# Kernel optimization log

Hardware: AMD Instinct MI355X
Metric: run time of the kernel (lower is better)

The kernel has to match this reference:

```python
import jax, jax.numpy as jnp
import numpy as np

INF = 1000000000000.0
HEAD_SIZE = 64
HEADS = 12
MAX_LENGTH = 512


def _rope_tables(dim, max_length):
    inv_freq = 1.0 / (10000.0 ** (jnp.arange(0, dim, 2, dtype=jnp.float32) / dim))
    t = jnp.arange(max_length, dtype=jnp.float32)
    freqs = t[:, None] * inv_freq[None, :]  # [L, dim/2]
    return jnp.sin(freqs), jnp.cos(freqs)


def _apply_rope(t, sin, cos):
    # t: [B, L, d]; sin/cos: [L, d/2]
    t1, t2 = t[..., 0::2], t[..., 1::2]
    out = jnp.stack([t1 * cos - t2 * sin, t1 * sin + t2 * cos], axis=-1)
    return out.reshape(t.shape)


def setup_inputs() -> dict:
    key = jax.random.key(0)
    k1, k2, k3, k4, k5 = jax.random.split(key, 5)
    B, L, H = 16, 512, 1024
    inputs = jax.random.normal(k1, (B, L, H), dtype=jnp.float32)
    attention_mask = jnp.ones((B, L), dtype=jnp.float32)
    s1 = 1.0 / np.sqrt(H)
    s2 = 1.0 / np.sqrt(HEAD_SIZE * 2)
    W1 = jax.random.normal(k2, (H, HEAD_SIZE * 2), dtype=jnp.float32) * s1
    b1 = jax.random.normal(k3, (HEAD_SIZE * 2,), dtype=jnp.float32) * s1
    W2 = jax.random.normal(k4, (HEAD_SIZE * 2, HEADS * 2), dtype=jnp.float32) * s2
    b2 = jax.random.normal(k5, (HEADS * 2,), dtype=jnp.float32) * s2
    return {"inputs": inputs, "attention_mask": attention_mask,
            "W1": W1, "b1": b1, "W2": W2, "b2": b2}


def reference(inputs, attention_mask, W1, b1, W2, b2):
    B, L, _ = inputs.shape
    x = inputs @ W1 + b1                      # [B, L, 2*head_size]
    qw, kw = x[..., 0::2], x[..., 1::2]        # [B, L, head_size] each
    sin, cos = _rope_tables(HEAD_SIZE, MAX_LENGTH)
    sin, cos = sin[:L], cos[:L]
    qw = _apply_rope(qw, sin, cos)
    kw = _apply_rope(kw, sin, cos)
    logits = jnp.einsum('bmd,bnd->bmn', qw, kw) / (HEAD_SIZE ** 0.5)  # [B, L, L]
    bias = jnp.swapaxes(x @ W2 + b2, 1, 2) / 2.0                       # [B, 2*heads, L]
    # logits[b,h,m,n] = score[b,m,n] + bias_even[b,h,n] + bias_odd[b,h,m]
    logits = logits[:, None] + bias[:, 0::2, None, :] + bias[:, 1::2, :, None]
    attn_mask = 1.0 - attention_mask[:, None, None, :] * attention_mask[:, None, :, None]
    logits = logits - attn_mask * INF
    tril = jnp.tril(jnp.ones((L, L), dtype=logits.dtype), k=-1)
    logits = logits - tril * INF
    return logits
```

## Files before the change

kernel.cpp:

```cpp
#include <hip/hip_runtime.h>
#include <hip/hip_bf16.h>

typedef short bf16x8 __attribute__((ext_vector_type(8)));
typedef float f32x4 __attribute__((ext_vector_type(4)));
typedef unsigned short u16;
typedef unsigned short u16x8 __attribute__((ext_vector_type(8)));

#define FINF 1.0e12f

__device__ __forceinline__ u16 f2b(float f) {
  union { float f; unsigned int u; } x; x.f = f;
  unsigned int r = x.u + 0x7fffu + ((x.u >> 16) & 1u);
  return (u16)(r >> 16);
}

__global__ __launch_bounds__(256) void k1_prep(
    const float* __restrict__ inputs, const float* __restrict__ W1,
    const float* __restrict__ b1, const float* __restrict__ W2,
    const float* __restrict__ b2,
    u16* __restrict__ qw, u16* __restrict__ kw,
    float* __restrict__ biasE, float* __restrict__ biasO) {
  __shared__ u16 Al[32 * 64];
  __shared__ u16 Wl[8192];
  __shared__ float xt[32 * 132];
  __shared__ float w2t[24 * 132];

  int t = threadIdx.x;
  int lane = t & 63, w = t >> 6;
  int r0 = blockIdx.x * 32;
  int b = r0 >> 9, l0 = r0 & 511;

  #pragma unroll
  for (int i = 0; i < 12; ++i) {
    int idx = t + i * 256;
    int k = idx / 24, c = idx - k * 24;
    w2t[c * 132 + k] = W2[idx];
  }

  f32x4 acc[4];
  #pragma unroll
  for (int nti = 0; nti < 4; ++nti) acc[nti] = (f32x4){0.f, 0.f, 0.f, 0.f};

  int wr = (w & 1) * 16;
  int wnt = (w >> 1) * 4;

  for (int ch = 0; ch < 16; ++ch) {
    {
      int row = t >> 3, ks8 = (t & 7) * 8;
      const float4* src =
          (const float4*)&inputs[(size_t)(r0 + row) * 1024 + ch * 64 + ks8];
      float4 f0 = src[0], f1 = src[1];
      u16x8 uv;
      uv[0] = f2b(f0.x); uv[1] = f2b(f0.y); uv[2] = f2b(f0.z); uv[3] = f2b(f0.w);
      uv[4] = f2b(f1.x); uv[5] = f2b(f1.y); uv[6] = f2b(f1.z); uv[7] = f2b(f1.w);
      int byt = (row * 128 + (t & 7) * 16) ^ ((row & 7) << 4);
      *(u16x8*)((char*)Al + byt) = uv;
    }
    #pragma unroll
    for (int i = 0; i < 4; ++i) {
      int f = t + i * 256;
      int ln = f & 15, hi = (f >> 4) & 3, ksnt = f >> 6;
      int ks = ksnt & 1, nt = ksnt >> 1;
      int c = nt * 16 + ln;
      int kb = ch * 64 + ks * 32 + hi * 8;
      u16x8 uv;
      #pragma unroll
      for (int ii = 0; ii < 8; ++ii) uv[ii] = f2b(W1[(size_t)(kb + ii) * 128 + c]);
      *(u16x8*)&Wl[ksnt * 512 + (hi * 16 + ln) * 8] = uv;
    }
    __syncthreads();
    int arow = wr + (lane & 15);
    int hi = lane >> 4;
    #pragma unroll
    for (int ks = 0; ks < 2; ++ks) {
      int cb = ks * 64 + hi * 16;
      bf16x8 a = *(const bf16x8*)((const char*)Al +
                                  ((arow * 128 + cb) ^ ((arow & 7) << 4)));
      #pragma unroll
      for (int nti = 0; nti < 4; ++nti) {
        int nt = wnt + nti;
        bf16x8 bb = *(const bf16x8*)&Wl[((nt * 2 + ks) * 64 + lane) * 8];
        acc[nti] = __builtin_amdgcn_mfma_f32_16x16x32_bf16(a, bb, acc[nti], 0, 0, 0);
      }
    }
    __syncthreads();
  }

  #pragma unroll
  for (int nti = 0; nti < 4; ++nti) {
    int c = (wnt + nti) * 16 + (lane & 15);
    float b1v = b1[c];
    #pragma unroll
    for (int r = 0; r < 4; ++r) {
      int row = wr + ((lane >> 4) << 2) + r;
      xt[row * 132 + c] = acc[nti][r] + b1v;
    }
  }
  __syncthreads();

  {
    int r = t >> 3, jb = (t & 7) * 4;
    int l = l0 + r;
    float fl = (float)l;
    u16x8 qv, kv;
    #pragma unroll
    for (int p = 0; p < 4; ++p) {
      int j = jb + p;
      float4 x4 = *(const float4*)&xt[r * 132 + 4 * j];
      float invf = exp2f(-0.4152410118609203f * (float)j);
      float ang = fl * invf;
      float rev = ang * 0.15915494309189535f;
      rev = rev - floorf(rev);
      float sv, cv;
      __sincosf(rev * 6.2831853071795864f, &sv, &cv);
      qv[2 * p] = f2b(x4.x * cv - x4.z * sv);
      qv[2 * p + 1] = f2b(x4.x * sv + x4.z * cv);
      kv[2 * p] = f2b(x4.y * cv - x4.w * sv);
      kv[2 * p + 1] = f2b(x4.y * sv + x4.w * cv);
    }
    size_t base = ((size_t)(b * 512 + l)) * 64 + jb * 2;
    *(u16x8*)&qw[base] = qv;
    *(u16x8*)&kw[base] = kv;
  }

  if (t < 192) {
    int c = t >> 3;
    int rg = (t & 7) * 4;
    float s0 = b2[c], s1 = s0, s2 = s0, s3 = s0;
    #pragma unroll
    for (int k4 = 0; k4 < 32; ++k4) {
      float4 wv = *(const float4*)&w2t[c * 132 + k4 * 4];
      float4 x0 = *(const float4*)&xt[(rg + 0) * 132 + k4 * 4];
      float4 x1 = *(const float4*)&xt[(rg + 1) * 132 + k4 * 4];
      float4 x2 = *(const float4*)&xt[(rg + 2) * 132 + k4 * 4];
      float4 x3 = *(const float4*)&xt[(rg + 3) * 132 + k4 * 4];
      s0 += x0.x * wv.x + x0.y * wv.y + x0.z * wv.z + x0.w * wv.w;
      s1 += x1.x * wv.x + x1.y * wv.y + x1.z * wv.z + x1.w * wv.w;
      s2 += x2.x * wv.x + x2.y * wv.y + x2.z * wv.z + x2.w * wv.w;
      s3 += x3.x * wv.x + x3.y * wv.y + x3.z * wv.z + x3.w * wv.w;
    }
    int h = c >> 1;
    size_t o = ((size_t)(b * 12 + h)) * 512 + l0 + rg;
    float4 sv = {s0 * 0.5f, s1 * 0.5f, s2 * 0.5f, s3 * 0.5f};
    if (c & 1) *(float4*)&biasO[o] = sv;
    else       *(float4*)&biasE[o] = sv;
  }
}

__global__ __launch_bounds__(256) void k2_main(
    const u16* __restrict__ qw, const u16* __restrict__ kw,
    const float* __restrict__ biasE, const float* __restrict__ biasO,
    const float* __restrict__ amask, float* __restrict__ out) {
  __shared__ char smem[24448];
  u16* Q = (u16*)smem;
  u16* K = (u16*)(smem + 8192);
  float* qkL = (float*)smem;
  float* BN = (float*)(smem + 17408);
  float* BM = (float*)(smem + 17408 + 3264);
  float* AMm = (float*)(smem + 17408 + 6528);
  float* AMn = AMm + 64;

  int t = threadIdx.x;
  int lane = t & 63, w = t >> 6;
  int n0 = blockIdx.x * 64, m0 = blockIdx.y * 64, b = blockIdx.z;
  bool skip = (m0 >= n0 + 64);

  if (!skip) {
    int row = t >> 2, sg = t & 3;
    const u16x8* qsrc = (const u16x8*)&qw[((size_t)(b * 512 + m0 + row)) * 64 + sg * 16];
    u16x8 q0 = qsrc[0], q1 = qsrc[1];
    const u16x8* ksrc = (const u16x8*)&kw[((size_t)(b * 512 + n0 + row)) * 64 + sg * 16];
    u16x8 k0v = ksrc[0], k1v = ksrc[1];
    int swz = (row & 7) << 4;
    int byt = row * 128 + sg * 32;
    *(u16x8*)((char*)Q + ((byt) ^ swz)) = q0;
    *(u16x8*)((char*)Q + ((byt + 16) ^ swz)) = q1;
    *(u16x8*)((char*)K + ((byt) ^ swz)) = k0v;
    *(u16x8*)((char*)K + ((byt + 16) ^ swz)) = k1v;
  }
  if (t < 192) {
    int h = t >> 4, kq = t & 15;
    *(float4*)&BN[h * 68 + kq * 4] =
        *(const float4*)&biasE[((size_t)(b * 12 + h)) * 512 + n0 + kq * 4];
    *(float4*)&BM[h * 68 + kq * 4] =
        *(const float4*)&biasO[((size_t)(b * 12 + h)) * 512 + m0 + kq * 4];
  } else if (t < 224) {
    int i = t - 192;
    if (i < 16) *(float4*)&AMm[i * 4] = *(const float4*)&amask[b * 512 + m0 + i * 4];
    else { int ii = i - 16; *(float4*)&AMn[ii * 4] = *(const float4*)&amask[b * 512 + n0 + ii * 4]; }
  }
  __syncthreads();

  if (!skip) {
    f32x4 acc[4];
    #pragma unroll
    for (int nt = 0; nt < 4; ++nt) acc[nt] = (f32x4){0.f, 0.f, 0.f, 0.f};
    int mrow = w * 16 + (lane & 15);
    int hi = lane >> 4;
    #pragma unroll
    for (int ks = 0; ks < 2; ++ks) {
      int cb = ks * 64 + hi * 16;
      bf16x8 a = *(const bf16x8*)((const char*)Q +
                                  ((mrow * 128 + cb) ^ ((mrow & 7) << 4)));
      #pragma unroll
      for (int nt = 0; nt < 4; ++nt) {
        int nr = nt * 16 + (lane & 15);
        bf16x8 bb = *(const bf16x8*)((const char*)K +
                                     ((nr * 128 + cb) ^ ((nr & 7) << 4)));
        acc[nt] = __builtin_amdgcn_mfma_f32_16x16x32_bf16(a, bb, acc[nt], 0, 0, 0);
      }
    }
    __syncthreads();
    #pragma unroll
    for (int nt = 0; nt < 4; ++nt)
      #pragma unroll
      for (int r = 0; r < 4; ++r)
        qkL[(w * 16 + hi * 4 + r) * 68 + nt * 16 + (lane & 15)] = acc[nt][r];
    __syncthreads();
  }

  int a15 = t & 15, mb = t >> 4;
  float amn0 = AMn[a15 * 4 + 0], amn1 = AMn[a15 * 4 + 1];
  float amn2 = AMn[a15 * 4 + 2], amn3 = AMn[a15 * 4 + 3];
  float vals[4][4];
  #pragma unroll
  for (int mi = 0; mi < 4; ++mi) {
    int m = mb + 16 * mi;
    int mg = m0 + m;
    float amm = AMm[m];
    int ng = n0 + a15 * 4;
    float p0 = (1.f - amm * amn0) * FINF + ((mg > ng + 0) ? FINF : 0.f);
    float p1 = (1.f - amm * amn1) * FINF + ((mg > ng + 1) ? FINF : 0.f);
    float p2 = (1.f - amm * amn2) * FINF + ((mg > ng + 2) ? FINF : 0.f);
    float p3 = (1.f - amm * amn3) * FINF + ((mg > ng + 3) ? FINF : 0.f);
    if (!skip) {
      float4 qk = *(const float4*)&qkL[m * 68 + a15 * 4];
      vals[mi][0] = qk.x * 0.125f - p0;
      vals[mi][1] = qk.y * 0.125f - p1;
      vals[mi][2] = qk.z * 0.125f - p2;
      vals[mi][3] = qk.w * 0.125f - p3;
    } else {
      vals[mi][0] = -p0; vals[mi][1] = -p1; vals[mi][2] = -p2; vals[mi][3] = -p3;
    }
  }

  size_t outbase = (size_t)(b * 12) * 262144 + (size_t)m0 * 512 + n0 + a15 * 4;
  #pragma unroll
  for (int h = 0; h < 12; ++h) {
    float4 bn = *(const float4*)&BN[h * 68 + a15 * 4];
    #pragma unroll
    for (int mi = 0; mi < 4; ++mi) {
      int m = mb + 16 * mi;
      float bm = BM[h * 68 + m];
      float4 v;
      v.x = vals[mi][0] + bn.x + bm;
      v.y = vals[mi][1] + bn.y + bm;
      v.z = vals[mi][2] + bn.z + bm;
      v.w = vals[mi][3] + bn.w + bm;
      *(float4*)&out[outbase + (size_t)h * 262144 + (size_t)m * 512] = v;
    }
  }
}

extern "C" void kernel_launch(void* const* d_in, const int* in_sizes, int n_in,
                              void* d_out, int out_size, void* d_ws, size_t ws_size,
                              hipStream_t stream) {
  const float* inputs = (const float*)d_in[0];
  const float* amask  = (const float*)d_in[1];
  const float* W1     = (const float*)d_in[2];
  const float* b1     = (const float*)d_in[3];
  const float* W2     = (const float*)d_in[4];
  const float* b2     = (const float*)d_in[5];
  float* out = (float*)d_out;

  char* ws = (char*)d_ws;
  u16* qw      = (u16*)(ws);
  u16* kw      = (u16*)(ws + (1u << 20));
  float* biasE = (float*)(ws + (2u << 20));
  float* biasO = (float*)(ws + (2u << 20) + 393216u);

  k1_prep<<<256, 256, 0, stream>>>(inputs, W1, b1, W2, b2, qw, kw, biasE, biasO);
  k2_main<<<dim3(8, 8, 16), 256, 0, stream>>>(qw, kw, biasE, biasO, amask, out);
}
```

Measured before the change: 61.94 us.

## Pre-pack W1 into bf16 MFMA fragments and load operands directly from global

Adds a small pre-kernel that converts W1 to bf16 and reorders it into the exact MFMA B-fragment layout. The projection kernel then drops its LDS staging and barriers, reading A fragments straight from global with in-register bf16 conversion and B fragments as contiguous 16-byte loads. This removes the per-block strided fp32 W1 reads and the repeated conversions, at the cost of an extra launch and global reads that are no longer shared through LDS.

Result: slower. 92.20 us (+48.9%).

```diff
diff --git a/kernel.cpp b/kernel.cpp
--- a/kernel.cpp
+++ b/kernel.cpp
@@ -14,14 +14,24 @@
   return (u16)(r >> 16);
 }
 
+__global__ __launch_bounds__(256) void k0_w1frag(const float* __restrict__ W1,
+                                                 u16* __restrict__ w1f) {
+  int idx = blockIdx.x * 256 + threadIdx.x;
+  int k = idx >> 7, c = idx & 127;
+  float v = W1[idx];
+  int chunk = k >> 6, kk = k & 63;
+  int ks = kk >> 5, km = kk & 31, kg = km >> 3, i = km & 7;
+  int nt = c >> 4, ln = c & 15;
+  int dst = chunk * 8192 + (nt * 2 + ks) * 512 + (kg * 16 + ln) * 8 + i;
+  w1f[dst] = f2b(v);
+}
+
 __global__ __launch_bounds__(256) void k1_prep(
-    const float* __restrict__ inputs, const float* __restrict__ W1,
+    const float* __restrict__ inputs, const u16* __restrict__ w1f,
     const float* __restrict__ b1, const float* __restrict__ W2,
     const float* __restrict__ b2,
     u16* __restrict__ qw, u16* __restrict__ kw,
     float* __restrict__ biasE, float* __restrict__ biasO) {
-  __shared__ u16 Al[32 * 64];
-  __shared__ u16 Wl[8192];
   __shared__ float xt[32 * 132];
   __shared__ float w2t[24 * 132];
 
@@ -37,53 +47,38 @@
     w2t[c * 132 + k] = W2[idx];
   }
 
-  f32x4 acc[4];
-  #pragma unroll
-  for (int nti = 0; nti < 4; ++nti) acc[nti] = (f32x4){0.f, 0.f, 0.f, 0.f};
-
   int wr = (w & 1) * 16;
   int wnt = (w >> 1) * 4;
 
+  f32x4 acc[4];
+  #pragma unroll
+  for (int nti = 0; nti < 4; ++nti) acc[nti] = (f32x4){0.f, 0.f, 0.f, 0.f};
+
+  const float* ap = &inputs[(size_t)(r0 + wr + (lane & 15)) * 1024 + ((lane >> 4) << 3)];
+  const u16* wp = &w1f[lane * 8];
+
+  #pragma unroll 4
   for (int ch = 0; ch < 16; ++ch) {
-    {
-      int row = t >> 3, ks8 = (t & 7) * 8;
-      const float4* src =
-          (const float4*)&inputs[(size_t)(r0 + row) * 1024 + ch * 64 + ks8];
-      float4 f0 = src[0], f1 = src[1];
-      u16x8 uv;
-      uv[0] = f2b(f0.x); uv[1] = f2b(f0.y); uv[2] = f2b(f0.z); uv[3] = f2b(f0.w);
-      uv[4] = f2b(f1.x); uv[5] = f2b(f1.y); uv[6] = f2b(f1.z); uv[7] = f2b(f1.w);
-      int byt = (row * 128 + (t & 7) * 16) ^ ((row & 7) << 4);
-      *(u16x8*)((char*)Al + byt) = uv;
-    }
-    #pragma unroll
-    for (int i = 0; i < 4; ++i) {
-      int f = t + i * 256;
-      int ln = f & 15, hi = (f >> 4) & 3, ksnt = f >> 6;
-      int ks = ksnt & 1, nt = ksnt >> 1;
-      int c = nt * 16 + ln;
-      int kb = ch * 64 + ks * 32 + hi * 8;
-      u16x8 uv;
-      #pragma unroll
-      for (int ii = 0; ii < 8; ++ii) uv[ii] = f2b(W1[(size_t)(kb + ii) * 128 + c]);
-      *(u16x8*)&Wl[ksnt * 512 + (hi * 16 + ln) * 8] = uv;
-    }
-    __syncthreads();
-    int arow = wr + (lane & 15);
-    int hi = lane >> 4;
+    bf16x8 af[2];
     #pragma unroll
     for (int ks = 0; ks < 2; ++ks) {
-      int cb = ks * 64 + hi * 16;
-      bf16x8 a = *(const bf16x8*)((const char*)Al +
-                                  ((arow * 128 + cb) ^ ((arow & 7) << 4)));
+      float4 f0 = *(const float4*)&ap[ch * 64 + ks * 32];
+      float4 f1 = *(const float4*)&ap[ch * 64 + ks * 32 + 4];
+      bf16x8 av;
+      av[0] = (short)f2b(f0.x); av[1] = (short)f2b(f0.y);
+      av[2] = (short)f2b(f0.z); av[3] = (short)f2b(f0.w);
+      av[4] = (short)f2b(f1.x); av[5] = (short)f2b(f1.y);
+      av[6] = (short)f2b(f1.z); av[7] = (short)f2b(f1.w);
+      af[ks] = av;
+    }
+    #pragma unroll
+    for (int ks = 0; ks < 2; ++ks) {
       #pragma unroll
       for (int nti = 0; nti < 4; ++nti) {
-        int nt = wnt + nti;
-        bf16x8 bb = *(const bf16x8*)&Wl[((nt * 2 + ks) * 64 + lane) * 8];
-        acc[nti] = __builtin_amdgcn_mfma_f32_16x16x32_bf16(a, bb, acc[nti], 0, 0, 0);
+        bf16x8 bb = *(const bf16x8*)&wp[ch * 8192 + ((wnt + nti) * 2 + ks) * 512];
+        acc[nti] = __builtin_amdgcn_mfma_f32_16x16x32_bf16(af[ks], bb, acc[nti], 0, 0, 0);
       }
     }
-    __syncthreads();
   }
 
   #pragma unroll
@@ -278,7 +273,9 @@
   u16* kw      = (u16*)(ws + (1u << 20));
   float* biasE = (float*)(ws + (2u << 20));
   float* biasO = (float*)(ws + (2u << 20) + 393216u);
-
-  k1_prep<<<256, 256, 0, stream>>>(inputs, W1, b1, W2, b2, qw, kw, biasE, biasO);
+  u16* w1f     = (u16*)(ws + (2u << 20) + 786432u);
+
+  k0_w1frag<<<512, 256, 0, stream>>>(W1, w1f);
+  k1_prep<<<256, 256, 0, stream>>>(inputs, w1f, b1, W2, b2, qw, kw, biasE, biasO);
   k2_main<<<dim3(8, 8, 16), 256, 0, stream>>>(qw, kw, biasE, biasO, amask, out);
 }
```
